# Optimization experiments

Measured on AMD Instinct MI355X. Metric: run time of the kernel, lower is better.

The kernel has to match this reference:

```python
import jax, jax.numpy as jnp
import numpy as np

N, D_MODEL, D_PE, H = 4096, 512, 16, 8


def setup_inputs() -> dict:
    key = jax.random.key(0)
    ks = jax.random.split(key, 6)
    s = 1.0 / np.sqrt(D_MODEL)
    return {
        "x": jax.random.normal(ks[0], (N, D_MODEL), dtype=jnp.float32),
        "pe": jax.random.normal(ks[1], (N, D_PE), dtype=jnp.float32),
        "w_qkv": jax.random.normal(ks[2], (D_MODEL, 3 * D_MODEL), dtype=jnp.float32) * s,
        "b_qkv": jnp.zeros((3 * D_MODEL,), dtype=jnp.float32),
        "w_pe": jax.random.normal(ks[3], (D_PE, H), dtype=jnp.float32) * (1.0 / np.sqrt(D_PE)),
        "b_pe": jnp.zeros((H,), dtype=jnp.float32),
        "w_out": jax.random.normal(ks[4], (D_MODEL, D_MODEL), dtype=jnp.float32) * s,
        "b_out": jnp.zeros((D_MODEL,), dtype=jnp.float32),
    }


def reference(x, pe, w_qkv, b_qkv, w_pe, b_pe, w_out, b_out):
    n, d = x.shape
    h = w_pe.shape[1]
    hd = d // h
    scale = hd ** -0.5

    qkv = (x @ w_qkv + b_qkv).reshape(n, 3, h, hd)  # [N,3,H,hd]
    q = jnp.transpose(qkv[:, 0], (1, 0, 2))  # [H,N,hd]
    k = jnp.transpose(qkv[:, 1], (1, 0, 2))
    v = jnp.transpose(qkv[:, 2], (1, 0, 2))

    pe_proj = pe @ w_pe + b_pe  # [N,H]
    # bias[h,i,j] = pe_proj[j,h] - pe_proj[i,h]  (matches torch unsqueeze/permute)
    pt = pe_proj.T  # [H,N]
    bias = pt[:, None, :] - pt[:, :, None]  # [H,N,N]

    scores = jnp.einsum('hnd,hmd->hnm', q, k) * scale + bias  # [H,N,N]
    attn = jax.nn.softmax(scores, axis=-1)
    out = jnp.einsum('hnm,hmd->hnd', attn, v)  # [H,N,hd]
    out = jnp.transpose(out, (1, 0, 2)).reshape(n, d)
    return out @ w_out + b_out
```

## Files before the change

kernel.cpp:

```cpp
#include <hip/hip_runtime.h>
#include <stdint.h>
#include <stddef.h>


typedef unsigned short u16;
typedef __attribute__((ext_vector_type(8))) short short8;
typedef __attribute__((ext_vector_type(8))) unsigned short us8;
typedef __attribute__((ext_vector_type(4))) unsigned short us4;
typedef __attribute__((ext_vector_type(4))) float floatx4;

__device__ __forceinline__ u16 f2b(float f) {
  union { float f; uint32_t u; } v; v.f = f;
  uint32_t u = v.u;
  return (u16)((u + 0x7fffu + ((u >> 16) & 1u)) >> 16);
}

__device__ __forceinline__ uint32_t pkbf16(float a, float b) {
  union { float f; uint32_t u; } x, y; x.f = a; y.f = b;
  return __builtin_amdgcn_perm(y.u + 0x8000u, x.u + 0x8000u, 0x07060302u);
}

#if __has_builtin(__builtin_amdgcn_exp2f)
__device__ __forceinline__ float fexp2(float x) { return __builtin_amdgcn_exp2f(x); }
#else
__device__ __forceinline__ float fexp2(float x) { return exp2f(x); }
#endif

__device__ __forceinline__ void gld16(const u16* g, u16* l) {
  __builtin_amdgcn_global_load_lds(
      (const __attribute__((address_space(1))) uint32_t*)(const void*)g,
      (__attribute__((address_space(3))) uint32_t*)(void*)l, 16, 0, 0);
}


__device__ __forceinline__ void tr_tile(const float* __restrict__ in,
                                        u16* __restrict__ out, int R, int C,
                                        int bx, int by, u16 (*tile)[33]) {
  int tx = threadIdx.x & 31, ty = threadIdx.x >> 5;
  int c0 = bx * 32, r0 = by * 32;
#pragma unroll
  for (int i = 0; i < 32; i += 8)
    tile[ty + i][tx] = f2b(in[(size_t)(r0 + ty + i) * C + c0 + tx]);
  __syncthreads();
#pragma unroll
  for (int i = 0; i < 32; i += 8)
    out[(size_t)(c0 + ty + i) * R + r0 + tx] = tile[tx][ty + i];
}

__global__ __launch_bounds__(256) void k_prep(
    const float* __restrict__ x, u16* __restrict__ xb,
    const float* __restrict__ w_qkv, u16* __restrict__ wqkvT,
    const float* __restrict__ w_out, u16* __restrict__ woutT,
    const float* __restrict__ pe, const float* __restrict__ w_pe,
    const float* __restrict__ b_pe, float* __restrict__ peT) {
  __shared__ u16 tile[32][33];
  int b = blockIdx.x;
  if (b < 2048) {
    int i = b * 256 + threadIdx.x;
    float4 v = ((const float4*)x)[i];
    uint2 o = make_uint2(pkbf16(v.x, v.y), pkbf16(v.z, v.w));
    ((uint2*)xb)[i] = o;
  } else if (b < 2816) {
    int idx = b - 2048;
    tr_tile(w_qkv, wqkvT, 512, 1536, idx % 48, idx / 48, tile);
  } else if (b < 3072) {
    int idx = b - 2816;
    tr_tile(w_out, woutT, 512, 512, idx % 16, idx / 16, tile);
  } else {
    int idx = (b - 3072) * 256 + threadIdx.x;
    int h = idx >> 12, n = idx & 4095;
    float acc = b_pe[h];
#pragma unroll
    for (int d = 0; d < 16; ++d) acc = fmaf(pe[n * 16 + d], w_pe[d * 8 + h], acc);
    peT[h * 4096 + n] = acc * 1.4426950408889634f - 16.0f;
  }
}


__global__ __launch_bounds__(256) void k_gemm_qkv(const u16* __restrict__ A,
                                                  const u16* __restrict__ Bt,
                                                  const float* __restrict__ bias,
                                                  u16* __restrict__ qk,
                                                  u16* __restrict__ vtp) {
  __shared__ __align__(16) u16 smem[12288];
  const int tid = threadIdx.x;
  const int lane = tid & 63, wave = tid >> 6;
  const int colx = lane & 15, quad = lane >> 4;
  const int m0 = blockIdx.y * 64, n0 = blockIdx.x * 128;
  const int wr = (wave >> 1) * 32, wc = (wave & 1) * 64;
  const int scA = (lane & 3) ^ ((lane >> 3) & 3);
  const int sx = (colx >> 1) & 3;
  const floatx4 fz = {0.f, 0.f, 0.f, 0.f};
  floatx4 acc[2][4];
#pragma unroll
  for (int i = 0; i < 2; ++i)
#pragma unroll
    for (int j = 0; j < 4; ++j) acc[i][j] = fz;

#define PREF_QKV(k0, b)                                                       \
  {                                                                           \
    int rowa = wave * 16 + (lane >> 2);                                       \
    gld16(&A[(size_t)(m0 + rowa) * 512 + (k0) + scA * 8],                     \
          &smem[(b) * 2048 + wave * 512 + lane * 8]);                         \
    _Pragma("unroll") for (int c = 0; c < 2; ++c) {                           \
      int rowb = wave * 32 + c * 16 + (lane >> 2);                            \
      gld16(&Bt[(size_t)(n0 + rowb) * 512 + (k0) + scA * 8],                  \
            &smem[4096 + (b) * 4096 + wave * 1024 + c * 512 + lane * 8]);     \
    }                                                                         \
  }

  PREF_QKV(0, 0);
  __syncthreads();
  for (int it = 0; it < 16; ++it) {
    int cur = it & 1;
    if (it < 15) PREF_QKV((it + 1) * 32, cur ^ 1);
    const u16* As = &smem[cur * 2048];
    const u16* Bs = &smem[4096 + cur * 4096];
    short8 af[2], bf[4];
#pragma unroll
    for (int i = 0; i < 2; ++i)
      af[i] = *(const short8*)&As[(wr + i * 16 + colx) * 32 + (quad ^ sx) * 8];
#pragma unroll
    for (int j = 0; j < 4; ++j)
      bf[j] = *(const short8*)&Bs[(wc + j * 16 + colx) * 32 + (quad ^ sx) * 8];
#pragma unroll
    for (int i = 0; i < 2; ++i)
#pragma unroll
      for (int j = 0; j < 4; ++j)
        acc[i][j] = __builtin_amdgcn_mfma_f32_16x16x32_bf16(af[i], bf[j], acc[i][j], 0, 0, 0);
    __syncthreads();
  }

  const bool isV = (blockIdx.x >= 8);
#pragma unroll
  for (int j = 0; j < 4; ++j) {
    int c = n0 + wc + j * 16 + colx;
    float bq = bias[c];
    if (!isV) {
#pragma unroll
      for (int i = 0; i < 2; ++i)
#pragma unroll
        for (int r = 0; r < 4; ++r) {
          int row = m0 + wr + i * 16 + quad * 4 + r;
          qk[(size_t)row * 1024 + c] = f2b(acc[i][j][r] + bq);
        }
    } else {
      int d = c - 1024;
#pragma unroll
      for (int i = 0; i < 2; ++i) {
        us4 o;
#pragma unroll
        for (int r = 0; r < 4; ++r) o[r] = f2b(acc[i][j][r] + bq);
        *(us4*)&vtp[(size_t)d * 4096 + m0 + wr + quad * 8 + i * 4] = o;
      }
    }
  }
#undef PREF_QKV
}


__global__ __launch_bounds__(256) void k_gemm_out(const u16* __restrict__ A,
                                                  const u16* __restrict__ Bt,
                                                  const float* __restrict__ bias,
                                                  float* __restrict__ Cout) {
  __shared__ __align__(16) u16 smem[8192];
  const int tid = threadIdx.x;
  const int lane = tid & 63, wave = tid >> 6;
  const int colx = lane & 15, quad = lane >> 4;
  const int m0 = blockIdx.y * 64, n0 = blockIdx.x * 64;
  const int wr = (wave >> 1) * 32, wc = (wave & 1) * 32;
  const int scA = (lane & 3) ^ ((lane >> 3) & 3);
  const int sx = (colx >> 1) & 3;
  const floatx4 fz = {0.f, 0.f, 0.f, 0.f};
  floatx4 acc[2][2];
#pragma unroll
  for (int i = 0; i < 2; ++i)
#pragma unroll
    for (int j = 0; j < 2; ++j) acc[i][j] = fz;

#define PREF_OUT(k0, b)                                                       \
  {                                                                           \
    int rowa = wave * 16 + (lane >> 2);                                       \
    gld16(&A[(size_t)(m0 + rowa) * 512 + (k0) + scA * 8],                     \
          &smem[(b) * 2048 + wave * 512 + lane * 8]);                         \
    gld16(&Bt[(size_t)(n0 + rowa) * 512 + (k0) + scA * 8],                    \
          &smem[4096 + (b) * 2048 + wave * 512 + lane * 8]);                  \
  }

  PREF_OUT(0, 0);
  __syncthreads();
  for (int it = 0; it < 16; ++it) {
    int cur = it & 1;
    if (it < 15) PREF_OUT((it + 1) * 32, cur ^ 1);
    const u16* As = &smem[cur * 2048];
    const u16* Bs = &smem[4096 + cur * 2048];
    short8 af[2], bf[2];
#pragma unroll
    for (int i = 0; i < 2; ++i)
      af[i] = *(const short8*)&As[(wr + i * 16 + colx) * 32 + (quad ^ sx) * 8];
#pragma unroll
    for (int j = 0; j < 2; ++j)
      bf[j] = *(const short8*)&Bs[(wc + j * 16 + colx) * 32 + (quad ^ sx) * 8];
#pragma unroll
    for (int i = 0; i < 2; ++i)
#pragma unroll
      for (int j = 0; j < 2; ++j)
        acc[i][j] = __builtin_amdgcn_mfma_f32_16x16x32_bf16(af[i], bf[j], acc[i][j], 0, 0, 0);
    __syncthreads();
  }
#pragma unroll
  for (int j = 0; j < 2; ++j) {
    int c = n0 + wc + j * 16 + colx;
    float bq = bias[c];
#pragma unroll
    for (int i = 0; i < 2; ++i)
#pragma unroll
      for (int r = 0; r < 4; ++r) {
        int row = m0 + wr + i * 16 + quad * 4 + r;
        Cout[(size_t)row * 512 + c] = acc[i][j][r] + bq;
      }
  }
#undef PREF_OUT
}


__global__ __launch_bounds__(512, 4) void k_flash(const u16* __restrict__ qk,
                                                  const u16* __restrict__ vt,
                                                  const float* __restrict__ peT,
                                                  u16* __restrict__ ao) {
  __shared__ __align__(16) u16 smem[37376];
  float* bufs = (float*)smem;
  u16* fin = smem;

  const int tid = threadIdx.x;
  const int lane = tid & 63, wave = tid >> 6;
  const int colx = lane & 15, quad = lane >> 4;
  const int ih = wave & 1, jq = wave >> 1;
  const int q0 = blockIdx.x * 64;
  const int h = blockIdx.y;
  const float sscale = 0.125f * 1.4426950408889634f;
  const floatx4 fz = {0.f, 0.f, 0.f, 0.f};

  const int scK = (lane & 7) ^ (lane >> 3);
  const int rV = wave * 8 + (lane >> 4);
  const int scV0 = (lane & 15) ^ (rV & 15);
  const int scV1 = (lane & 15) ^ ((rV + 4) & 15);

#define PREF_F(j0n, b)                                                        \
  {                                                                           \
    _Pragma("unroll") for (int c = 0; c < 2; ++c) {                           \
      int row = wave * 16 + c * 8 + (lane >> 3);                              \
      gld16(&qk[(size_t)((j0n) + row) * 1024 + 512 + h * 64 + scK * 8],       \
            &smem[4096 + (b) * 8192 + wave * 1024 + c * 512 + lane * 8]);     \
    }                                                                         \
    gld16(&vt[(size_t)(h * 64 + rV) * 4096 + (j0n) + scV0 * 8],               \
          &smem[20480 + (b) * 8192 + wave * 1024 + lane * 8]);                \
    gld16(&vt[(size_t)(h * 64 + rV + 4) * 4096 + (j0n) + scV1 * 8],           \
          &smem[20480 + (b) * 8192 + wave * 1024 + 512 + lane * 8]);          \
    if (tid < 128)                                                            \
      ((float*)(smem + 36864 + (b) * 256))[tid] = peT[h * 4096 + (j0n) + tid];\
  }

  {
    int row = tid >> 3, ch = tid & 7;
    int slot = ch ^ (row & 7);
    *(us8*)&smem[row * 64 + slot * 8] =
        *(const us8*)&qk[(size_t)(q0 + row) * 1024 + h * 64 + ch * 8];
  }
  PREF_F(0, 0);
  __syncthreads();

  short8 qf[2][2];
#pragma unroll
  for (int i2 = 0; i2 < 2; ++i2)
#pragma unroll
    for (int kk = 0; kk < 2; ++kk) {
      int row = ih * 32 + i2 * 16 + colx;
      qf[i2][kk] = *(const short8*)&smem[row * 64 + ((kk * 4 + quad) ^ (colx & 7)) * 8];
    }

  floatx4 oacc[2][4];
  float rsum[2] = {0.0f, 0.0f};
#pragma unroll
  for (int i2 = 0; i2 < 2; ++i2)
#pragma unroll
    for (int cb = 0; cb < 4; ++cb) oacc[i2][cb] = fz;

  for (int it = 0; it < 32; ++it) {
    const int cur = it & 1;
    if (it < 31) PREF_F((it + 1) * 128, cur ^ 1);

    const u16* Ks = &smem[4096 + cur * 8192];
    const u16* Vts = &smem[20480 + cur * 8192];
    const float* pes = (const float*)(smem + 36864 + cur * 256);

    short8 kf[2][2];
#pragma unroll
    for (int j2 = 0; j2 < 2; ++j2)
#pragma unroll
      for (int kk = 0; kk < 2; ++kk) {
        int row = jq * 32 + j2 * 16 + colx;
        kf[j2][kk] = *(const short8*)&Ks[row * 64 + ((kk * 4 + quad) ^ (colx & 7)) * 8];
      }
    short8 vf[4];
#pragma unroll
    for (int cb = 0; cb < 4; ++cb) {
      int row = cb * 16 + colx;
      vf[cb] = *(const short8*)&Vts[row * 128 + ((jq * 4 + quad) ^ colx) * 8];
    }
    floatx4 pev[2];
#pragma unroll
    for (int j2 = 0; j2 < 2; ++j2)
      pev[j2] = *(const floatx4*)&pes[jq * 32 + j2 * 16 + quad * 4];

#pragma unroll
    for (int i2 = 0; i2 < 2; ++i2) {
      floatx4 sacc[2] = {fz, fz};
#pragma unroll
      for (int j2 = 0; j2 < 2; ++j2)
#pragma unroll
        for (int kk = 0; kk < 2; ++kk)
          sacc[j2] = __builtin_amdgcn_mfma_f32_16x16x32_bf16(kf[j2][kk], qf[i2][kk], sacc[j2], 0, 0, 0);
      union { uint32_t w[4]; short8 s; } pk;
#pragma unroll
      for (int j2 = 0; j2 < 2; ++j2) {
        float p0 = fexp2(fmaf(sacc[j2][0], sscale, pev[j2][0]));
        float p1 = fexp2(fmaf(sacc[j2][1], sscale, pev[j2][1]));
        float p2 = fexp2(fmaf(sacc[j2][2], sscale, pev[j2][2]));
        float p3 = fexp2(fmaf(sacc[j2][3], sscale, pev[j2][3]));
        rsum[i2] += (p0 + p1) + (p2 + p3);
        pk.w[j2 * 2 + 0] = pkbf16(p0, p1);
        pk.w[j2 * 2 + 1] = pkbf16(p2, p3);
      }
#pragma unroll
      for (int cb = 0; cb < 4; ++cb)
        oacc[i2][cb] = __builtin_amdgcn_mfma_f32_16x16x32_bf16(pk.s, vf[cb], oacc[i2][cb], 0, 0, 0);
    }
    __syncthreads();
  }

  floatx4 lacc[2];
#pragma unroll
  for (int i2 = 0; i2 < 2; ++i2) {
    rsum[i2] += __shfl_xor(rsum[i2], 16);
    rsum[i2] += __shfl_xor(rsum[i2], 32);
#pragma unroll
    for (int r = 0; r < 4; ++r) lacc[i2][r] = __shfl(rsum[i2], quad * 4 + r, 16);
  }

  float* s0 = bufs + (0 * 2 + ih) * 2080;
  float* s1 = bufs + (1 * 2 + ih) * 2080;
  if (jq >= 2) {
    float* b = (jq == 2) ? s0 : s1;
#pragma unroll
    for (int i2 = 0; i2 < 2; ++i2) {
#pragma unroll
      for (int cb = 0; cb < 4; ++cb)
#pragma unroll
        for (int r = 0; r < 4; ++r)
          b[(i2 * 16 + quad * 4 + r) * 65 + cb * 16 + colx] = oacc[i2][cb][r];
      if (colx == 0)
#pragma unroll
        for (int r = 0; r < 4; ++r)
          b[(i2 * 16 + quad * 4 + r) * 65 + 64] = lacc[i2][r];
    }
  }
  __syncthreads();
  if (jq < 2) {
    float* b = (jq == 0) ? s0 : s1;
#pragma unroll
    for (int i2 = 0; i2 < 2; ++i2) {
#pragma unroll
      for (int cb = 0; cb < 4; ++cb)
#pragma unroll
        for (int r = 0; r < 4; ++r)
          oacc[i2][cb][r] += b[(i2 * 16 + quad * 4 + r) * 65 + cb * 16 + colx];
#pragma unroll
      for (int r = 0; r < 4; ++r)
        lacc[i2][r] += b[(i2 * 16 + quad * 4 + r) * 65 + 64];
    }
  }
  __syncthreads();
  if (jq == 1) {
#pragma unroll
    for (int i2 = 0; i2 < 2; ++i2) {
#pragma unroll
      for (int cb = 0; cb < 4; ++cb)
#pragma unroll
        for (int r = 0; r < 4; ++r)
          s1[(i2 * 16 + quad * 4 + r) * 65 + cb * 16 + colx] = oacc[i2][cb][r];
      if (colx == 0)
#pragma unroll
        for (int r = 0; r < 4; ++r)
          s1[(i2 * 16 + quad * 4 + r) * 65 + 64] = lacc[i2][r];
    }
  }
  __syncthreads();
  if (jq == 0) {
#pragma unroll
    for (int i2 = 0; i2 < 2; ++i2) {
#pragma unroll
      for (int cb = 0; cb < 4; ++cb)
#pragma unroll
        for (int r = 0; r < 4; ++r)
          oacc[i2][cb][r] += s1[(i2 * 16 + quad * 4 + r) * 65 + cb * 16 + colx];
#pragma unroll
      for (int r = 0; r < 4; ++r)
        lacc[i2][r] += s1[(i2 * 16 + quad * 4 + r) * 65 + 64];
#pragma unroll
      for (int r = 0; r < 4; ++r) {
        float inv = 1.0f / lacc[i2][r];
#pragma unroll
        for (int cb = 0; cb < 4; ++cb)
          fin[(ih * 32 + i2 * 16 + quad * 4 + r) * 68 + cb * 16 + colx] =
              f2b(oacc[i2][cb][r] * inv);
      }
    }
  }
  __syncthreads();
  {
    int row = tid >> 3, ch = tid & 7;
    *(us8*)&ao[(size_t)(q0 + row) * 512 + h * 64 + ch * 8] =
        *(const us8*)&fin[row * 68 + ch * 8];
  }
#undef PREF_F
}


extern "C" void kernel_launch(void* const* d_in, const int* in_sizes, int n_in,
                              void* d_out, int out_size, void* d_ws, size_t ws_size,
                              hipStream_t stream) {
  const float* x     = (const float*)d_in[0];
  const float* pe    = (const float*)d_in[1];
  const float* w_qkv = (const float*)d_in[2];
  const float* b_qkv = (const float*)d_in[3];
  const float* w_pe  = (const float*)d_in[4];
  const float* b_pe  = (const float*)d_in[5];
  const float* w_out = (const float*)d_in[6];
  const float* b_out = (const float*)d_in[7];
  float* out = (float*)d_out;

  u16* xb    = (u16*)d_ws;
  u16* wqkvT = xb    + 2097152;
  u16* woutT = wqkvT + 786432;
  u16* qk    = woutT + 262144;
  u16* vt    = qk    + 4194304;
  u16* ao    = vt    + 2097152;
  float* peT = (float*)(ao + 2097152);

  k_prep<<<3200, 256, 0, stream>>>(x, xb, w_qkv, wqkvT, w_out, woutT,
                                   pe, w_pe, b_pe, peT);
  k_gemm_qkv<<<dim3(12, 64), 256, 0, stream>>>(xb, wqkvT, b_qkv, qk, vt);
  k_flash<<<dim3(64, 8), 512, 0, stream>>>(qk, vt, peT, ao);
  k_gemm_out<<<dim3(8, 64), 256, 0, stream>>>(ao, woutT, b_out, out);
}
```

Baseline: 149.2 us.

## Split attention over KV halves with a combine kernel; widen GEMM blocks to 8 waves

The flash kernel now splits the key/value range into two halves via a third grid dimension. Each block handles 16 query rows per wave pair with smaller tiles and reads the positional bias straight from global memory. It writes unnormalized partial outputs and row sums to a workspace, and a new combine kernel sums the halves, normalizes and converts to bf16. Both projection GEMMs move to 512-thread blocks with a 64-wide K step and a new swizzle. This adds parallelism and occupancy, at the cost of extra fp32 partial traffic and one more launch.

```diff
diff --git a/kernel.cpp b/kernel.cpp
--- a/kernel.cpp
+++ b/kernel.cpp
@@ -77,71 +77,77 @@
 }
 
 
-__global__ __launch_bounds__(256) void k_gemm_qkv(const u16* __restrict__ A,
-                                                  const u16* __restrict__ Bt,
-                                                  const float* __restrict__ bias,
-                                                  u16* __restrict__ qk,
-                                                  u16* __restrict__ vtp) {
-  __shared__ __align__(16) u16 smem[12288];
+__global__ __launch_bounds__(512, 6) void k_gemm_qkv(const u16* __restrict__ A,
+                                                     const u16* __restrict__ Bt,
+                                                     const float* __restrict__ bias,
+                                                     u16* __restrict__ qk,
+                                                     u16* __restrict__ vtp) {
+  __shared__ __align__(16) u16 smem[24576];
   const int tid = threadIdx.x;
   const int lane = tid & 63, wave = tid >> 6;
   const int colx = lane & 15, quad = lane >> 4;
   const int m0 = blockIdx.y * 64, n0 = blockIdx.x * 128;
-  const int wr = (wave >> 1) * 32, wc = (wave & 1) * 64;
-  const int scA = (lane & 3) ^ ((lane >> 3) & 3);
-  const int sx = (colx >> 1) & 3;
+  const int wm = wave >> 2, wn = wave & 3;
+  const int sc = (lane & 7) ^ ((lane >> 3) & 7);
   const floatx4 fz = {0.f, 0.f, 0.f, 0.f};
-  floatx4 acc[2][4];
+  floatx4 acc[2][2];
 #pragma unroll
   for (int i = 0; i < 2; ++i)
 #pragma unroll
-    for (int j = 0; j < 4; ++j) acc[i][j] = fz;
+    for (int j = 0; j < 2; ++j) acc[i][j] = fz;
 
 #define PREF_QKV(k0, b)                                                       \
   {                                                                           \
-    int rowa = wave * 16 + (lane >> 2);                                       \
-    gld16(&A[(size_t)(m0 + rowa) * 512 + (k0) + scA * 8],                     \
-          &smem[(b) * 2048 + wave * 512 + lane * 8]);                         \
+    int rowa = wave * 8 + (lane >> 3);                                        \
+    gld16(&A[(size_t)(m0 + rowa) * 512 + (k0) + sc * 8],                      \
+          &smem[(b) * 4096 + wave * 512 + lane * 8]);                         \
     _Pragma("unroll") for (int c = 0; c < 2; ++c) {                           \
-      int rowb = wave * 32 + c * 16 + (lane >> 2);                            \
-      gld16(&Bt[(size_t)(n0 + rowb) * 512 + (k0) + scA * 8],                  \
-            &smem[4096 + (b) * 4096 + wave * 1024 + c * 512 + lane * 8]);     \
+      int rowb = wave * 16 + c * 8 + (lane >> 3);                             \
+      gld16(&Bt[(size_t)(n0 + rowb) * 512 + (k0) + sc * 8],                   \
+            &smem[8192 + (b) * 8192 + wave * 1024 + c * 512 + lane * 8]);     \
     }                                                                         \
   }
 
   PREF_QKV(0, 0);
   __syncthreads();
-  for (int it = 0; it < 16; ++it) {
+  for (int it = 0; it < 8; ++it) {
     int cur = it & 1;
-    if (it < 15) PREF_QKV((it + 1) * 32, cur ^ 1);
-    const u16* As = &smem[cur * 2048];
-    const u16* Bs = &smem[4096 + cur * 4096];
-    short8 af[2], bf[4];
-#pragma unroll
-    for (int i = 0; i < 2; ++i)
-      af[i] = *(const short8*)&As[(wr + i * 16 + colx) * 32 + (quad ^ sx) * 8];
-#pragma unroll
-    for (int j = 0; j < 4; ++j)
-      bf[j] = *(const short8*)&Bs[(wc + j * 16 + colx) * 32 + (quad ^ sx) * 8];
-#pragma unroll
-    for (int i = 0; i < 2; ++i)
-#pragma unroll
-      for (int j = 0; j < 4; ++j)
-        acc[i][j] = __builtin_amdgcn_mfma_f32_16x16x32_bf16(af[i], bf[j], acc[i][j], 0, 0, 0);
+    if (it < 7) PREF_QKV((it + 1) * 64, cur ^ 1);
+    const u16* As = &smem[cur * 4096];
+    const u16* Bs = &smem[8192 + cur * 8192];
+#pragma unroll
+    for (int kk = 0; kk < 2; ++kk) {
+      short8 af[2], bf[2];
+#pragma unroll
+      for (int i = 0; i < 2; ++i) {
+        int row = wm * 32 + i * 16 + colx;
+        af[i] = *(const short8*)&As[row * 64 + (((kk * 4 + quad) ^ (colx & 7))) * 8];
+      }
+#pragma unroll
+      for (int j = 0; j < 2; ++j) {
+        int row = wn * 32 + j * 16 + colx;
+        bf[j] = *(const short8*)&Bs[row * 64 + (((kk * 4 + quad) ^ (colx & 7))) * 8];
+      }
+#pragma unroll
+      for (int i = 0; i < 2; ++i)
+#pragma unroll
+        for (int j = 0; j < 2; ++j)
+          acc[i][j] = __builtin_amdgcn_mfma_f32_16x16x32_bf16(af[i], bf[j], acc[i][j], 0, 0, 0);
+    }
     __syncthreads();
   }
 
   const bool isV = (blockIdx.x >= 8);
 #pragma unroll
-  for (int j = 0; j < 4; ++j) {
-    int c = n0 + wc + j * 16 + colx;
+  for (int j = 0; j < 2; ++j) {
+    int c = n0 + wn * 32 + j * 16 + colx;
     float bq = bias[c];
     if (!isV) {
 #pragma unroll
       for (int i = 0; i < 2; ++i)
 #pragma unroll
         for (int r = 0; r < 4; ++r) {
-          int row = m0 + wr + i * 16 + quad * 4 + r;
+          int row = m0 + wm * 32 + i * 16 + quad * 4 + r;
           qk[(size_t)row * 1024 + c] = f2b(acc[i][j][r] + bq);
         }
     } else {
@@ -151,7 +157,7 @@
         us4 o;
 #pragma unroll
         for (int r = 0; r < 4; ++r) o[r] = f2b(acc[i][j][r] + bq);
-        *(us4*)&vtp[(size_t)d * 4096 + m0 + wr + quad * 8 + i * 4] = o;
+        *(us4*)&vtp[(size_t)d * 4096 + m0 + wm * 32 + quad * 8 + i * 4] = o;
       }
     }
   }
@@ -159,271 +165,209 @@
 }
 
 
-__global__ __launch_bounds__(256) void k_gemm_out(const u16* __restrict__ A,
-                                                  const u16* __restrict__ Bt,
-                                                  const float* __restrict__ bias,
-                                                  float* __restrict__ Cout) {
-  __shared__ __align__(16) u16 smem[8192];
+__global__ __launch_bounds__(512, 4) void k_gemm_out(const u16* __restrict__ A,
+                                                     const u16* __restrict__ Bt,
+                                                     const float* __restrict__ bias,
+                                                     float* __restrict__ Cout) {
+  __shared__ __align__(16) u16 smem[16384];
   const int tid = threadIdx.x;
   const int lane = tid & 63, wave = tid >> 6;
   const int colx = lane & 15, quad = lane >> 4;
   const int m0 = blockIdx.y * 64, n0 = blockIdx.x * 64;
-  const int wr = (wave >> 1) * 32, wc = (wave & 1) * 32;
-  const int scA = (lane & 3) ^ ((lane >> 3) & 3);
-  const int sx = (colx >> 1) & 3;
+  const int wm = wave >> 2, wn = wave & 3;
+  const int sc = (lane & 7) ^ ((lane >> 3) & 7);
   const floatx4 fz = {0.f, 0.f, 0.f, 0.f};
-  floatx4 acc[2][2];
-#pragma unroll
-  for (int i = 0; i < 2; ++i)
-#pragma unroll
-    for (int j = 0; j < 2; ++j) acc[i][j] = fz;
+  floatx4 acc[2];
+  acc[0] = fz; acc[1] = fz;
 
 #define PREF_OUT(k0, b)                                                       \
   {                                                                           \
-    int rowa = wave * 16 + (lane >> 2);                                       \
-    gld16(&A[(size_t)(m0 + rowa) * 512 + (k0) + scA * 8],                     \
-          &smem[(b) * 2048 + wave * 512 + lane * 8]);                         \
-    gld16(&Bt[(size_t)(n0 + rowa) * 512 + (k0) + scA * 8],                    \
-          &smem[4096 + (b) * 2048 + wave * 512 + lane * 8]);                  \
+    int rowa = wave * 8 + (lane >> 3);                                        \
+    gld16(&A[(size_t)(m0 + rowa) * 512 + (k0) + sc * 8],                      \
+          &smem[(b) * 4096 + wave * 512 + lane * 8]);                         \
+    gld16(&Bt[(size_t)(n0 + rowa) * 512 + (k0) + sc * 8],                     \
+          &smem[8192 + (b) * 4096 + wave * 512 + lane * 8]);                  \
   }
 
   PREF_OUT(0, 0);
   __syncthreads();
-  for (int it = 0; it < 16; ++it) {
+  for (int it = 0; it < 8; ++it) {
     int cur = it & 1;
-    if (it < 15) PREF_OUT((it + 1) * 32, cur ^ 1);
-    const u16* As = &smem[cur * 2048];
-    const u16* Bs = &smem[4096 + cur * 2048];
-    short8 af[2], bf[2];
-#pragma unroll
-    for (int i = 0; i < 2; ++i)
-      af[i] = *(const short8*)&As[(wr + i * 16 + colx) * 32 + (quad ^ sx) * 8];
-#pragma unroll
-    for (int j = 0; j < 2; ++j)
-      bf[j] = *(const short8*)&Bs[(wc + j * 16 + colx) * 32 + (quad ^ sx) * 8];
-#pragma unroll
-    for (int i = 0; i < 2; ++i)
-#pragma unroll
-      for (int j = 0; j < 2; ++j)
-        acc[i][j] = __builtin_amdgcn_mfma_f32_16x16x32_bf16(af[i], bf[j], acc[i][j], 0, 0, 0);
+    if (it < 7) PREF_OUT((it + 1) * 64, cur ^ 1);
+    const u16* As = &smem[cur * 4096];
+    const u16* Bs = &smem[8192 + cur * 4096];
+#pragma unroll
+    for (int kk = 0; kk < 2; ++kk) {
+      short8 af[2], bf;
+#pragma unroll
+      for (int i = 0; i < 2; ++i) {
+        int row = wm * 32 + i * 16 + colx;
+        af[i] = *(const short8*)&As[row * 64 + (((kk * 4 + quad) ^ (colx & 7))) * 8];
+      }
+      {
+        int row = wn * 16 + colx;
+        bf = *(const short8*)&Bs[row * 64 + (((kk * 4 + quad) ^ (colx & 7))) * 8];
+      }
+#pragma unroll
+      for (int i = 0; i < 2; ++i)
+        acc[i] = __builtin_amdgcn_mfma_f32_16x16x32_bf16(af[i], bf, acc[i], 0, 0, 0);
+    }
     __syncthreads();
   }
-#pragma unroll
-  for (int j = 0; j < 2; ++j) {
-    int c = n0 + wc + j * 16 + colx;
-    float bq = bias[c];
-#pragma unroll
-    for (int i = 0; i < 2; ++i)
-#pragma unroll
-      for (int r = 0; r < 4; ++r) {
-        int row = m0 + wr + i * 16 + quad * 4 + r;
-        Cout[(size_t)row * 512 + c] = acc[i][j][r] + bq;
-      }
-  }
+  int c = n0 + wn * 16 + colx;
+  float bq = bias[c];
+#pragma unroll
+  for (int i = 0; i < 2; ++i)
+#pragma unroll
+    for (int r = 0; r < 4; ++r) {
+      int row = m0 + wm * 32 + i * 16 + quad * 4 + r;
+      Cout[(size_t)row * 512 + c] = acc[i][r] + bq;
+    }
 #undef PREF_OUT
 }
 
 
-__global__ __launch_bounds__(512, 4) void k_flash(const u16* __restrict__ qk,
+__global__ __launch_bounds__(512, 8) void k_flash(const u16* __restrict__ qk,
                                                   const u16* __restrict__ vt,
                                                   const float* __restrict__ peT,
-                                                  u16* __restrict__ ao) {
-  __shared__ __align__(16) u16 smem[37376];
+                                                  float* __restrict__ opart,
+                                                  float* __restrict__ lpart) {
+  __shared__ __align__(16) u16 smem[20480];
   float* bufs = (float*)smem;
-  u16* fin = smem;
 
   const int tid = threadIdx.x;
   const int lane = tid & 63, wave = tid >> 6;
   const int colx = lane & 15, quad = lane >> 4;
-  const int ih = wave & 1, jq = wave >> 1;
+  const int ih = wave >> 1, jq = wave & 1;
   const int q0 = blockIdx.x * 64;
   const int h = blockIdx.y;
+  const int z = blockIdx.z;
+  const int kvb = z * 2048;
   const float sscale = 0.125f * 1.4426950408889634f;
   const floatx4 fz = {0.f, 0.f, 0.f, 0.f};
 
-  const int scK = (lane & 7) ^ (lane >> 3);
-  const int rV = wave * 8 + (lane >> 4);
-  const int scV0 = (lane & 15) ^ (rV & 15);
-  const int scV1 = (lane & 15) ^ ((rV + 4) & 15);
+  const int sc = (lane & 7) ^ ((lane >> 3) & 7);
+  const int srow = wave * 8 + (lane >> 3);
 
 #define PREF_F(j0n, b)                                                        \
   {                                                                           \
-    _Pragma("unroll") for (int c = 0; c < 2; ++c) {                           \
-      int row = wave * 16 + c * 8 + (lane >> 3);                              \
-      gld16(&qk[(size_t)((j0n) + row) * 1024 + 512 + h * 64 + scK * 8],       \
-            &smem[4096 + (b) * 8192 + wave * 1024 + c * 512 + lane * 8]);     \
-    }                                                                         \
-    gld16(&vt[(size_t)(h * 64 + rV) * 4096 + (j0n) + scV0 * 8],               \
-          &smem[20480 + (b) * 8192 + wave * 1024 + lane * 8]);                \
-    gld16(&vt[(size_t)(h * 64 + rV + 4) * 4096 + (j0n) + scV1 * 8],           \
-          &smem[20480 + (b) * 8192 + wave * 1024 + 512 + lane * 8]);          \
-    if (tid < 128)                                                            \
-      ((float*)(smem + 36864 + (b) * 256))[tid] = peT[h * 4096 + (j0n) + tid];\
+    gld16(&qk[(size_t)(kvb + (j0n) + srow) * 1024 + 512 + h * 64 + sc * 8],   \
+          &smem[4096 + (b) * 4096 + wave * 512 + lane * 8]);                  \
+    gld16(&vt[(size_t)(h * 64 + srow) * 4096 + kvb + (j0n) + sc * 8],         \
+          &smem[12288 + (b) * 4096 + wave * 512 + lane * 8]);                 \
   }
 
   {
     int row = tid >> 3, ch = tid & 7;
-    int slot = ch ^ (row & 7);
-    *(us8*)&smem[row * 64 + slot * 8] =
+    *(us8*)&smem[row * 64 + (ch ^ (row & 7)) * 8] =
         *(const us8*)&qk[(size_t)(q0 + row) * 1024 + h * 64 + ch * 8];
   }
   PREF_F(0, 0);
   __syncthreads();
 
-  short8 qf[2][2];
-#pragma unroll
-  for (int i2 = 0; i2 < 2; ++i2)
-#pragma unroll
-    for (int kk = 0; kk < 2; ++kk) {
-      int row = ih * 32 + i2 * 16 + colx;
-      qf[i2][kk] = *(const short8*)&smem[row * 64 + ((kk * 4 + quad) ^ (colx & 7)) * 8];
-    }
-
-  floatx4 oacc[2][4];
-  float rsum[2] = {0.0f, 0.0f};
-#pragma unroll
-  for (int i2 = 0; i2 < 2; ++i2)
-#pragma unroll
-    for (int cb = 0; cb < 4; ++cb) oacc[i2][cb] = fz;
+  short8 qf[2];
+#pragma unroll
+  for (int kk = 0; kk < 2; ++kk) {
+    int row = ih * 16 + colx;
+    qf[kk] = *(const short8*)&smem[row * 64 + (((kk * 4 + quad) ^ (colx & 7))) * 8];
+  }
+
+  floatx4 oacc[4];
+#pragma unroll
+  for (int cb = 0; cb < 4; ++cb) oacc[cb] = fz;
+  float rsum = 0.0f;
 
   for (int it = 0; it < 32; ++it) {
     const int cur = it & 1;
-    if (it < 31) PREF_F((it + 1) * 128, cur ^ 1);
-
-    const u16* Ks = &smem[4096 + cur * 8192];
-    const u16* Vts = &smem[20480 + cur * 8192];
-    const float* pes = (const float*)(smem + 36864 + cur * 256);
-
-    short8 kf[2][2];
+    if (it < 31) PREF_F((it + 1) * 64, cur ^ 1);
+    const u16* Ks = &smem[4096 + cur * 4096];
+    const u16* Vts = &smem[12288 + cur * 4096];
+
+    floatx4 pev[2];
 #pragma unroll
     for (int j2 = 0; j2 < 2; ++j2)
+      pev[j2] = *(const floatx4*)&peT[h * 4096 + kvb + it * 64 + jq * 32 + j2 * 16 + quad * 4];
+
+    floatx4 sacc[2] = {fz, fz};
+#pragma unroll
+    for (int j2 = 0; j2 < 2; ++j2) {
 #pragma unroll
       for (int kk = 0; kk < 2; ++kk) {
         int row = jq * 32 + j2 * 16 + colx;
-        kf[j2][kk] = *(const short8*)&Ks[row * 64 + ((kk * 4 + quad) ^ (colx & 7)) * 8];
-      }
-    short8 vf[4];
+        short8 kf = *(const short8*)&Ks[row * 64 + (((kk * 4 + quad) ^ (colx & 7))) * 8];
+        sacc[j2] = __builtin_amdgcn_mfma_f32_16x16x32_bf16(kf, qf[kk], sacc[j2], 0, 0, 0);
+      }
+    }
+    union { uint32_t w[4]; short8 s; } pk;
+#pragma unroll
+    for (int j2 = 0; j2 < 2; ++j2) {
+      float p0 = fexp2(fmaf(sacc[j2][0], sscale, pev[j2][0]));
+      float p1 = fexp2(fmaf(sacc[j2][1], sscale, pev[j2][1]));
+      float p2 = fexp2(fmaf(sacc[j2][2], sscale, pev[j2][2]));
+      float p3 = fexp2(fmaf(sacc[j2][3], sscale, pev[j2][3]));
+      rsum += (p0 + p1) + (p2 + p3);
+      pk.w[j2 * 2 + 0] = pkbf16(p0, p1);
+      pk.w[j2 * 2 + 1] = pkbf16(p2, p3);
+    }
 #pragma unroll
     for (int cb = 0; cb < 4; ++cb) {
       int row = cb * 16 + colx;
-      vf[cb] = *(const short8*)&Vts[row * 128 + ((jq * 4 + quad) ^ colx) * 8];
-    }
-    floatx4 pev[2];
-#pragma unroll
-    for (int j2 = 0; j2 < 2; ++j2)
-      pev[j2] = *(const floatx4*)&pes[jq * 32 + j2 * 16 + quad * 4];
-
-#pragma unroll
-    for (int i2 = 0; i2 < 2; ++i2) {
-      floatx4 sacc[2] = {fz, fz};
-#pragma unroll
-      for (int j2 = 0; j2 < 2; ++j2)
-#pragma unroll
-        for (int kk = 0; kk < 2; ++kk)
-          sacc[j2] = __builtin_amdgcn_mfma_f32_16x16x32_bf16(kf[j2][kk], qf[i2][kk], sacc[j2], 0, 0, 0);
-      union { uint32_t w[4]; short8 s; } pk;
-#pragma unroll
-      for (int j2 = 0; j2 < 2; ++j2) {
-        float p0 = fexp2(fmaf(sacc[j2][0], sscale, pev[j2][0]));
-        float p1 = fexp2(fmaf(sacc[j2][1], sscale, pev[j2][1]));
-        float p2 = fexp2(fmaf(sacc[j2][2], sscale, pev[j2][2]));
-        float p3 = fexp2(fmaf(sacc[j2][3], sscale, pev[j2][3]));
-        rsum[i2] += (p0 + p1) + (p2 + p3);
-        pk.w[j2 * 2 + 0] = pkbf16(p0, p1);
-        pk.w[j2 * 2 + 1] = pkbf16(p2, p3);
-      }
-#pragma unroll
-      for (int cb = 0; cb < 4; ++cb)
-        oacc[i2][cb] = __builtin_amdgcn_mfma_f32_16x16x32_bf16(pk.s, vf[cb], oacc[i2][cb], 0, 0, 0);
+      short8 vf = *(const short8*)&Vts[row * 64 + (((jq * 4 + quad) ^ (colx & 7))) * 8];
+      oacc[cb] = __builtin_amdgcn_mfma_f32_16x16x32_bf16(pk.s, vf, oacc[cb], 0, 0, 0);
     }
     __syncthreads();
   }
 
-  floatx4 lacc[2];
-#pragma unroll
-  for (int i2 = 0; i2 < 2; ++i2) {
-    rsum[i2] += __shfl_xor(rsum[i2], 16);
-    rsum[i2] += __shfl_xor(rsum[i2], 32);
-#pragma unroll
-    for (int r = 0; r < 4; ++r) lacc[i2][r] = __shfl(rsum[i2], quad * 4 + r, 16);
-  }
-
-  float* s0 = bufs + (0 * 2 + ih) * 2080;
-  float* s1 = bufs + (1 * 2 + ih) * 2080;
-  if (jq >= 2) {
-    float* b = (jq == 2) ? s0 : s1;
-#pragma unroll
-    for (int i2 = 0; i2 < 2; ++i2) {
-#pragma unroll
-      for (int cb = 0; cb < 4; ++cb)
-#pragma unroll
-        for (int r = 0; r < 4; ++r)
-          b[(i2 * 16 + quad * 4 + r) * 65 + cb * 16 + colx] = oacc[i2][cb][r];
-      if (colx == 0)
-#pragma unroll
-        for (int r = 0; r < 4; ++r)
-          b[(i2 * 16 + quad * 4 + r) * 65 + 64] = lacc[i2][r];
-    }
-  }
-  __syncthreads();
-  if (jq < 2) {
-    float* b = (jq == 0) ? s0 : s1;
-#pragma unroll
-    for (int i2 = 0; i2 < 2; ++i2) {
-#pragma unroll
-      for (int cb = 0; cb < 4; ++cb)
-#pragma unroll
-        for (int r = 0; r < 4; ++r)
-          oacc[i2][cb][r] += b[(i2 * 16 + quad * 4 + r) * 65 + cb * 16 + colx];
+  rsum += __shfl_xor(rsum, 16);
+  rsum += __shfl_xor(rsum, 32);
+
+  float* b = bufs + ih * 1040;
+  if (jq == 1) {
+#pragma unroll
+    for (int cb = 0; cb < 4; ++cb)
 #pragma unroll
       for (int r = 0; r < 4; ++r)
-        lacc[i2][r] += b[(i2 * 16 + quad * 4 + r) * 65 + 64];
-    }
-  }
-  __syncthreads();
-  if (jq == 1) {
-#pragma unroll
-    for (int i2 = 0; i2 < 2; ++i2) {
-#pragma unroll
-      for (int cb = 0; cb < 4; ++cb)
-#pragma unroll
-        for (int r = 0; r < 4; ++r)
-          s1[(i2 * 16 + quad * 4 + r) * 65 + cb * 16 + colx] = oacc[i2][cb][r];
-      if (colx == 0)
-#pragma unroll
-        for (int r = 0; r < 4; ++r)
-          s1[(i2 * 16 + quad * 4 + r) * 65 + 64] = lacc[i2][r];
-    }
+        b[(quad * 4 + r) * 65 + cb * 16 + colx] = oacc[cb][r];
+    if (quad == 0) b[colx * 65 + 64] = rsum;
   }
   __syncthreads();
   if (jq == 0) {
 #pragma unroll
-    for (int i2 = 0; i2 < 2; ++i2) {
-#pragma unroll
-      for (int cb = 0; cb < 4; ++cb)
-#pragma unroll
-        for (int r = 0; r < 4; ++r)
-          oacc[i2][cb][r] += s1[(i2 * 16 + quad * 4 + r) * 65 + cb * 16 + colx];
+    for (int cb = 0; cb < 4; ++cb)
 #pragma unroll
       for (int r = 0; r < 4; ++r)
-        lacc[i2][r] += s1[(i2 * 16 + quad * 4 + r) * 65 + 64];
-#pragma unroll
-      for (int r = 0; r < 4; ++r) {
-        float inv = 1.0f / lacc[i2][r];
-#pragma unroll
-        for (int cb = 0; cb < 4; ++cb)
-          fin[(ih * 32 + i2 * 16 + quad * 4 + r) * 68 + cb * 16 + colx] =
-              f2b(oacc[i2][cb][r] * inv);
-      }
-    }
-  }
-  __syncthreads();
-  {
-    int row = tid >> 3, ch = tid & 7;
-    *(us8*)&ao[(size_t)(q0 + row) * 512 + h * 64 + ch * 8] =
-        *(const us8*)&fin[row * 68 + ch * 8];
+        oacc[cb][r] += b[(quad * 4 + r) * 65 + cb * 16 + colx];
+    rsum += b[colx * 65 + 64];
+    float* op = opart + (size_t)z * 2097152;
+#pragma unroll
+    for (int cb = 0; cb < 4; ++cb)
+#pragma unroll
+      for (int r = 0; r < 4; ++r)
+        op[(size_t)(q0 + ih * 16 + quad * 4 + r) * 512 + h * 64 + cb * 16 + colx] =
+            oacc[cb][r];
+    if (quad == 0)
+      lpart[z * 32768 + h * 4096 + q0 + ih * 16 + colx] = rsum;
   }
 #undef PREF_F
+}
+
+
+__global__ __launch_bounds__(256) void k_comb(const float* __restrict__ opart,
+                                              const float* __restrict__ lpart,
+                                              u16* __restrict__ ao) {
+  int idx = blockIdx.x * 256 + threadIdx.x;
+  int n = idx >> 7, d4 = idx & 127;
+  int h = d4 >> 4;
+  float l = lpart[h * 4096 + n] + lpart[32768 + h * 4096 + n];
+  float inv = 1.0f / l;
+  float4 o0 = *(const float4*)&opart[(size_t)n * 512 + d4 * 4];
+  float4 o1 = *(const float4*)&opart[2097152 + (size_t)n * 512 + d4 * 4];
+  us4 o;
+  o[0] = f2b((o0.x + o1.x) * inv);
+  o[1] = f2b((o0.y + o1.y) * inv);
+  o[2] = f2b((o0.z + o1.z) * inv);
+  o[3] = f2b((o0.w + o1.w) * inv);
+  *(us4*)&ao[(size_t)n * 512 + d4 * 4] = o;
 }
 
 
@@ -446,11 +390,14 @@
   u16* qk    = woutT + 262144;
   u16* vt    = qk    + 4194304;
   u16* ao    = vt    + 2097152;
-  float* peT = (float*)(ao + 2097152);
+  float* peT   = (float*)(ao + 2097152);
+  float* opart = peT + 32768;
+  float* lpart = opart + 4194304;
 
   k_prep<<<3200, 256, 0, stream>>>(x, xb, w_qkv, wqkvT, w_out, woutT,
                                    pe, w_pe, b_pe, peT);
-  k_gemm_qkv<<<dim3(12, 64), 256, 0, stream>>>(xb, wqkvT, b_qkv, qk, vt);
-  k_flash<<<dim3(64, 8), 512, 0, stream>>>(qk, vt, peT, ao);
-  k_gemm_out<<<dim3(8, 64), 256, 0, stream>>>(ao, woutT, b_out, out);
-}
+  k_gemm_qkv<<<dim3(12, 64), 512, 0, stream>>>(xb, wqkvT, b_qkv, qk, vt);
+  k_flash<<<dim3(64, 8, 2), 512, 0, stream>>>(qk, vt, peT, opart, lpart);
+  k_comb<<<2048, 256, 0, stream>>>(opart, lpart, ao);
+  k_gemm_out<<<dim3(8, 64), 512, 0, stream>>>(ao, woutT, b_out, out);
+}
```

New measurement: 152.5 us. 1.02x slower.
